# Kernel optimization log

Hardware: AMD Instinct MI355X
Metric: run time of the kernel (lower is better)

Reference implementation:

```python
import jax, jax.numpy as jnp
import numpy as np
import math

B, T, C, H = 4, 2048, 1024, 16
D = C // H  # head dim = 64
W_STD = 0.02


def setup_inputs() -> dict:
    key = jax.random.key(0)
    kx, kw, kb = jax.random.split(key, 3)
    x = jax.random.normal(kx, (B, T, C), dtype=jnp.float32)
    # Linear params stored as [in, 3*in] for x @ W; scaled like typical init
    w_qkv = jax.random.normal(kw, (C, 3 * C), dtype=jnp.float32) * W_STD
    b_qkv = jax.random.normal(kb, (3 * C,), dtype=jnp.float32) * W_STD
    return {"x": x, "w_qkv": w_qkv, "b_qkv": b_qkv}


def reference(x, w_qkv, b_qkv):
    # Fused QKV projection; torch splits as keys, queries, values (in that order)
    qkv = x @ w_qkv + b_qkv                      # [B, T, 3C]
    k, q, v = jnp.split(qkv, 3, axis=-1)          # each [B, T, C]

    def heads(t):  # [B, T, C] -> [B, H, T, D]
        return t.reshape(B, T, H, D).transpose(0, 2, 1, 3)

    k, q, v = heads(k), heads(q), heads(v)
    scale = 1.0 / math.sqrt(D)
    logits = jnp.einsum("bhqd,bhkd->bhqk", q, k) * scale  # [B, H, T, T]
    causal = jnp.tril(jnp.ones((T, T), dtype=bool))
    logits = jnp.where(causal, logits, -jnp.inf)
    probs = jax.nn.softmax(logits, axis=-1)
    y = jnp.einsum("bhqk,bhkd->bhqd", probs, v)   # [B, H, T, D]
    return y.transpose(0, 2, 1, 3).reshape(B, T, C)
```

## Files before the change

### kernel.cpp

```cpp
#include <hip/hip_runtime.h>
#include <hip/hip_bf16.h>

typedef unsigned short ushort_t;
typedef __attribute__((ext_vector_type(4))) short bf16x4_t;
typedef __attribute__((ext_vector_type(8))) short short8;
typedef __attribute__((ext_vector_type(4))) unsigned short ushort4_t;
typedef __attribute__((ext_vector_type(4))) float f32x4;
typedef __attribute__((ext_vector_type(2))) unsigned int uint2_t;
typedef __attribute__((ext_vector_type(4))) unsigned int uint4_t;

#define LOG2E 1.44269504088896340736f

__device__ __forceinline__ unsigned short f2bf(float f) {
    unsigned int u = __float_as_uint(f);
    u += 0x7fffu + ((u >> 16) & 1u);
    return (unsigned short)(u >> 16);
}

__device__ __forceinline__ unsigned int pk2bf(float a, float b) {
    union { __hip_bfloat162 h2; unsigned int u; } cvt;
    cvt.h2 = __float22bfloat162_rn(make_float2(a, b));
    return cvt.u;
}

__device__ __forceinline__ void gl_lds16(const ushort_t* g, ushort_t* l) {
    __builtin_amdgcn_global_load_lds(
        (const __attribute__((address_space(1))) unsigned int*)g,
        (__attribute__((address_space(3))) unsigned int*)l, 16, 0, 0);
}

__device__ __forceinline__ f32x4 mfma16(uint2_t a, uint2_t b, f32x4 c) {
    union { uint2_t u; bf16x4_t s; } ua, ub;
    ua.u = a; ub.u = b;
    return __builtin_amdgcn_mfma_f32_16x16x16bf16_1k(ua.s, ub.s, c, 0, 0, 0);
}

__global__ __launch_bounds__(256) void cvt_x(
    const float* __restrict__ x, ushort_t* __restrict__ xb)
{
    const size_t i = ((size_t)blockIdx.x * 256 + threadIdx.x) * 8;
    const float4 a = *(const float4*)(x + i);
    const float4 b = *(const float4*)(x + i + 4);
    uint4_t o;
    o[0] = pk2bf(a.x, a.y); o[1] = pk2bf(a.z, a.w);
    o[2] = pk2bf(b.x, b.y); o[3] = pk2bf(b.z, b.w);
    *(uint4_t*)(xb + i) = o;
}

__global__ __launch_bounds__(256) void cvt_w(
    const float* __restrict__ w, ushort_t* __restrict__ wt)
{
    __shared__ ushort_t Ts[64][40];
    const int k0 = blockIdx.x * 32, n0 = blockIdx.y * 64;
    const int tid = threadIdx.x;
    const int kr = tid >> 3, nc = (tid & 7) * 8;
    const float* g = w + (size_t)(k0 + kr) * 3072 + n0 + nc;
    const float4 a = *(const float4*)g;
    const float4 b = *(const float4*)(g + 4);
    const float vals[8] = {a.x, a.y, a.z, a.w, b.x, b.y, b.z, b.w};
#pragma unroll
    for (int j = 0; j < 8; ++j) Ts[nc + j][kr] = f2bf(vals[j]);
    __syncthreads();
    const int nr = tid >> 2, kc = (tid & 3) * 8;
    const short8 v = *(const short8*)&Ts[nr][kc];
    *(short8*)(wt + (size_t)(n0 + nr) * 1024 + k0 + kc) = v;
}

__global__ __launch_bounds__(256) void qkv_gemm(
    const ushort_t* __restrict__ xb, const ushort_t* __restrict__ wt,
    const float* __restrict__ bq,
    ushort_t* __restrict__ kws, ushort_t* __restrict__ qws,
    ushort_t* __restrict__ vws)
{
    __shared__ ushort_t As[128 * 32];
    __shared__ ushort_t Bs[128 * 32];

    const int tid  = threadIdx.x;
    const int m0   = blockIdx.x * 128;
    const int n0   = blockIdx.y * 128;
    const int wv   = tid >> 6;
    const int lane = tid & 63;
    const int qr   = lane & 15;
    const int quad = lane >> 4;
    const int wm   = (wv >> 1) * 64;
    const int wn   = (wv & 1) * 64;

    const int lr   = lane >> 2;
    const int scol = (lane & 3) * 8;
    const ushort_t* gA = xb + (size_t)(m0 + wv*32 + lr) * 1024 + scol;
    const ushort_t* gB = wt + (size_t)(n0 + wv*32 + lr) * 1024 + scol;
    ushort_t* lA = As + wv * 32 * 32;
    ushort_t* lB = Bs + wv * 32 * 32;

    f32x4 acc[4][4];
#pragma unroll
    for (int i = 0; i < 4; ++i)
#pragma unroll
        for (int j = 0; j < 4; ++j) acc[i][j] = (f32x4){0.f, 0.f, 0.f, 0.f};

    for (int k0 = 0; k0 < 1024; k0 += 32) {
        __syncthreads();
        gl_lds16(gA + k0,             lA);
        gl_lds16(gA + k0 + 16 * 1024, lA + 16 * 32);
        gl_lds16(gB + k0,             lB);
        gl_lds16(gB + k0 + 16 * 1024, lB + 16 * 32);
        __syncthreads();

        short8 af[4], bfr[4];
#pragma unroll
        for (int i = 0; i < 4; ++i)
            af[i] = *(const short8*)&As[(wm + i*16 + qr) * 32 + quad * 8];
#pragma unroll
        for (int j = 0; j < 4; ++j)
            bfr[j] = *(const short8*)&Bs[(wn + j*16 + qr) * 32 + quad * 8];
#pragma unroll
        for (int i = 0; i < 4; ++i)
#pragma unroll
            for (int j = 0; j < 4; ++j)
                acc[i][j] = __builtin_amdgcn_mfma_f32_16x16x32_bf16(
                    af[i], bfr[j], acc[i][j], 0, 0, 0);
    }

    const int nbase = n0 + wn;
    const int sec   = nbase >> 10;
    const int h     = (nbase & 1023) >> 6;

    if (sec == 2) {
#pragma unroll
        for (int j = 0; j < 4; ++j) {
            const float bias = bq[nbase + j*16 + qr];
            const int d = j*16 + qr;
#pragma unroll
            for (int i = 0; i < 4; ++i) {
                const int m  = m0 + wm + i*16 + quad*4;
                const int bb = m >> 11;
                const int tt = m & 2047;
                ushort4_t pk;
#pragma unroll
                for (int r = 0; r < 4; ++r) pk[r] = f2bf(acc[i][j][r] + bias);
                *(ushort4_t*)&vws[((size_t)(bb*16 + h)*64 + d)*2048 + tt] = pk;
            }
        }
    } else {
        ushort_t* __restrict__ dst = (sec == 0) ? kws : qws;
#pragma unroll
        for (int j = 0; j < 4; ++j) {
            const float bias = bq[nbase + j*16 + qr];
            const int d = j*16 + qr;
#pragma unroll
            for (int i = 0; i < 4; ++i) {
#pragma unroll
                for (int r = 0; r < 4; ++r) {
                    const int m  = m0 + wm + i*16 + quad*4 + r;
                    const int bb = m >> 11;
                    const int tt = m & 2047;
                    dst[(((size_t)(bb*16 + h)) * 2048 + tt) * 64 + d] =
                        f2bf(acc[i][j][r] + bias);
                }
            }
        }
    }
}

__global__ __launch_bounds__(256) void attn_fwd(
    const ushort_t* __restrict__ kws, const ushort_t* __restrict__ qws,
    const ushort_t* __restrict__ vws, float* __restrict__ out,
    unsigned int* __restrict__ counter)
{
    constexpr int LDK = 72;
    __shared__ ushort_t Ks[2][64 * LDK];
    __shared__ ushort_t Vs[2][64 * LDK];
    __shared__ int s_item;

    const int tid  = threadIdx.x;
    const int wv   = tid >> 6;
    const int lane = tid & 63;
    const int qr   = lane & 15;
    const int quad = lane >> 4;
    const int srow = tid >> 2;
    const int scol = (tid & 3) * 16;
    constexpr float SCL = 0.125f * LOG2E;
    constexpr float CB  = 8.0f;

    for (;;) {
        if (tid == 0) s_item = (int)atomicAdd(counter, 1u);
        __syncthreads();
        const int item = s_item;
        if (item >= 1024) break;

        const int qt = 15 - (item >> 6);
        const int bh = item & 63;
        const int q0 = qt * 128;
        const size_t bhT = (size_t)bh * 2048;
        const ushort_t* kbase = kws + bhT * 64;
        const ushort_t* vbase = vws + (size_t)bh * 64 * 2048;

        const int base = q0 + wv*32;
        const int qv0 = base + qr;
        const int qv1 = qv0 + 16;

        const ushort_t* qg0 = qws + (bhT + qv0) * 64;
        const ushort_t* qg1 = qws + (bhT + qv1) * 64;
        const short8 Qb00 = *(const short8*)(qg0 + quad*8);
        const short8 Qb01 = *(const short8*)(qg0 + 32 + quad*8);
        const short8 Qb10 = *(const short8*)(qg1 + quad*8);
        const short8 Qb11 = *(const short8*)(qg1 + 32 + quad*8);

        float l_s[2] = {0.f, 0.f};
        f32x4 Oacc[2][4];
#pragma unroll
        for (int qs = 0; qs < 2; ++qs)
#pragma unroll
            for (int dt = 0; dt < 4; ++dt) Oacc[qs][dt] = (f32x4){0.f,0.f,0.f,0.f};

        const int nkt = 2*qt + 2;
        const int row_max = base + 31;

        short8 kv0, kv1, vv0, vv1;
        {
            const ushort_t* kg = kbase + (size_t)srow * 64 + scol;
            const ushort_t* vg = vbase + (size_t)srow * 2048 + scol;
            kv0 = *(const short8*)(kg);     kv1 = *(const short8*)(kg + 8);
            vv0 = *(const short8*)(vg);     vv1 = *(const short8*)(vg + 8);
        }
        *(short8*)&Ks[0][srow * LDK + scol]     = kv0;
        *(short8*)&Ks[0][srow * LDK + scol + 8] = kv1;
        *(short8*)&Vs[0][srow * LDK + scol]     = vv0;
        *(short8*)&Vs[0][srow * LDK + scol + 8] = vv1;
        __syncthreads();

        for (int kt = 0; kt < nkt; ++kt) {
            const int k0 = kt * 64;
            const int cur = kt & 1;
            const bool more = (kt + 1 < nkt);
            if (more) {
                const ushort_t* kg = kbase + (size_t)(k0 + 64 + srow) * 64 + scol;
                const ushort_t* vg = vbase + (size_t)srow * 2048 + k0 + 64 + scol;
                kv0 = *(const short8*)(kg);   kv1 = *(const short8*)(kg + 8);
                vv0 = *(const short8*)(vg);   vv1 = *(const short8*)(vg + 8);
            }

            if (k0 <= row_max) {
                const ushort_t* Kc = Ks[cur];
                const ushort_t* Vc = Vs[cur];
                const bool diag = (k0 + 63 > base);

                uint2_t pks[2][4];
                float ps0 = 0.f, ps1 = 0.f;
#pragma unroll
                for (int t4 = 0; t4 < 4; ++t4) {
                    const short8 kf0 = *(const short8*)&Kc[(t4*16 + qr)*LDK + quad*8];
                    const short8 kf1 = *(const short8*)&Kc[(t4*16 + qr)*LDK + 32 + quad*8];
                    f32x4 a = (f32x4){0.f,0.f,0.f,0.f};
                    f32x4 b = (f32x4){0.f,0.f,0.f,0.f};
                    a = __builtin_amdgcn_mfma_f32_16x16x32_bf16(kf0, Qb00, a, 0,0,0);
                    a = __builtin_amdgcn_mfma_f32_16x16x32_bf16(kf1, Qb01, a, 0,0,0);
                    b = __builtin_amdgcn_mfma_f32_16x16x32_bf16(kf0, Qb10, b, 0,0,0);
                    b = __builtin_amdgcn_mfma_f32_16x16x32_bf16(kf1, Qb11, b, 0,0,0);
                    if (diag) {
#pragma unroll
                        for (int r = 0; r < 4; ++r) {
                            const int key = k0 + t4*16 + quad*4 + r;
                            if (key > qv0) a[r] = -INFINITY;
                            if (key > qv1) b[r] = -INFINITY;
                        }
                    }
                    float p0[4], p1[4];
#pragma unroll
                    for (int r = 0; r < 4; ++r) {
                        p0[r] = exp2f(__builtin_fmaf(a[r], SCL, -CB));
                        p1[r] = exp2f(__builtin_fmaf(b[r], SCL, -CB));
                        ps0 += p0[r];
                        ps1 += p1[r];
                    }
                    pks[0][t4][0] = pk2bf(p0[0], p0[1]);
                    pks[0][t4][1] = pk2bf(p0[2], p0[3]);
                    pks[1][t4][0] = pk2bf(p1[0], p1[1]);
                    pks[1][t4][1] = pk2bf(p1[2], p1[3]);
                }
                l_s[0] += ps0;
                l_s[1] += ps1;

#pragma unroll
                for (int dt = 0; dt < 4; ++dt) {
#pragma unroll
                    for (int t4 = 0; t4 < 4; ++t4) {
                        const uint2_t vf = *(const uint2_t*)
                            &Vc[(dt*16 + qr)*LDK + t4*16 + quad*4];
                        Oacc[0][dt] = mfma16(pks[0][t4], vf, Oacc[0][dt]);
                        Oacc[1][dt] = mfma16(pks[1][t4], vf, Oacc[1][dt]);
                    }
                }
            }

            if (more) {
                ushort_t* Kn = Ks[cur ^ 1];
                ushort_t* Vn = Vs[cur ^ 1];
                *(short8*)&Kn[srow * LDK + scol]     = kv0;
                *(short8*)&Kn[srow * LDK + scol + 8] = kv1;
                *(short8*)&Vn[srow * LDK + scol]     = vv0;
                *(short8*)&Vn[srow * LDK + scol + 8] = vv1;
            }
            __syncthreads();
        }

        const int b = bh >> 4, h = bh & 15;
#pragma unroll
        for (int qs = 0; qs < 2; ++qs) {
            float lf = l_s[qs];
            lf += __shfl_xor(lf, 16);
            lf += __shfl_xor(lf, 32);
#pragma unroll
            for (int r = 0; r < 4; ++r) {
                const float lr  = __shfl(lf, quad*4 + r);
                const float inv = 1.f / lr;
                const int q = q0 + wv*32 + qs*16 + quad*4 + r;
                float* o = out + ((size_t)(b*2048 + q)) * 1024 + h*64;
#pragma unroll
                for (int dt = 0; dt < 4; ++dt) o[dt*16 + qr] = Oacc[qs][dt][r] * inv;
            }
        }
    }
}

extern "C" void kernel_launch(void* const* d_in, const int* in_sizes, int n_in,
                              void* d_out, int out_size, void* d_ws, size_t ws_size,
                              hipStream_t stream) {
    (void)in_sizes; (void)n_in; (void)out_size; (void)ws_size;
    const float* x  = (const float*)d_in[0];
    const float* w  = (const float*)d_in[1];
    const float* bq = (const float*)d_in[2];
    float* out = (float*)d_out;

    ushort_t* kws = (ushort_t*)d_ws;
    ushort_t* qws = kws + (size_t)8388608;
    ushort_t* vws = qws + (size_t)8388608;
    ushort_t* xb  = vws + (size_t)8388608;
    ushort_t* wt  = xb  + (size_t)8388608;
    unsigned int* counter = (unsigned int*)(wt + (size_t)3145728);

    (void)hipMemsetAsync(counter, 0, 4, stream);
    cvt_x<<<4096, 256, 0, stream>>>(x, xb);
    cvt_w<<<dim3(32, 48), 256, 0, stream>>>(w, wt);
    qkv_gemm<<<dim3(64, 24), 256, 0, stream>>>(xb, wt, bq, kws, qws, vws);
    attn_fwd<<<1024, 256, 0, stream>>>(kws, qws, vws, out, counter);
}
```

Baseline: 264.0 us.

## Replace atomic work queue with static paired causal tiles per block

The attention kernel no longer pulls work items from an atomic counter. Each of 512 blocks statically handles two query tiles (jp and 15-jp) of one batch-head, so every block gets the same causal workload. This drops the memset, the per-item atomic and the barrier, and may improve K/V cache locality within a head. In exchange there is no dynamic balancing, and with 512 equal blocks the tail depends on how they map onto the CUs.

Result: faster. 248.3 us (-5.9%).

```diff
diff --git a/kernel.cpp b/kernel.cpp
--- a/kernel.cpp
+++ b/kernel.cpp
@@ -164,13 +164,11 @@
 
 __global__ __launch_bounds__(256) void attn_fwd(
     const ushort_t* __restrict__ kws, const ushort_t* __restrict__ qws,
-    const ushort_t* __restrict__ vws, float* __restrict__ out,
-    unsigned int* __restrict__ counter)
+    const ushort_t* __restrict__ vws, float* __restrict__ out)
 {
     constexpr int LDK = 72;
     __shared__ ushort_t Ks[2][64 * LDK];
     __shared__ ushort_t Vs[2][64 * LDK];
-    __shared__ int s_item;
 
     const int tid  = threadIdx.x;
     const int wv   = tid >> 6;
@@ -182,18 +180,17 @@
     constexpr float SCL = 0.125f * LOG2E;
     constexpr float CB  = 8.0f;
 
-    for (;;) {
-        if (tid == 0) s_item = (int)atomicAdd(counter, 1u);
-        __syncthreads();
-        const int item = s_item;
-        if (item >= 1024) break;
-
-        const int qt = 15 - (item >> 6);
-        const int bh = item & 63;
+    const int bh = (int)blockIdx.x >> 3;
+    const int jp = (int)blockIdx.x & 7;
+    const size_t bhT = (size_t)bh * 2048;
+    const ushort_t* kbase = kws + bhT * 64;
+    const ushort_t* vbase = vws + (size_t)bh * 64 * 2048;
+    const int b = bh >> 4, h = bh & 15;
+
+#pragma unroll 1
+    for (int part = 0; part < 2; ++part) {
+        const int qt = part ? (15 - jp) : jp;
         const int q0 = qt * 128;
-        const size_t bhT = (size_t)bh * 2048;
-        const ushort_t* kbase = kws + bhT * 64;
-        const ushort_t* vbase = vws + (size_t)bh * 64 * 2048;
 
         const int base = q0 + wv*32;
         const int qv0 = base + qr;
@@ -252,24 +249,24 @@
                     const short8 kf0 = *(const short8*)&Kc[(t4*16 + qr)*LDK + quad*8];
                     const short8 kf1 = *(const short8*)&Kc[(t4*16 + qr)*LDK + 32 + quad*8];
                     f32x4 a = (f32x4){0.f,0.f,0.f,0.f};
-                    f32x4 b = (f32x4){0.f,0.f,0.f,0.f};
-                    a = __builtin_amdgcn_mfma_f32_16x16x32_bf16(kf0, Qb00, a, 0,0,0);
-                    a = __builtin_amdgcn_mfma_f32_16x16x32_bf16(kf1, Qb01, a, 0,0,0);
-                    b = __builtin_amdgcn_mfma_f32_16x16x32_bf16(kf0, Qb10, b, 0,0,0);
-                    b = __builtin_amdgcn_mfma_f32_16x16x32_bf16(kf1, Qb11, b, 0,0,0);
+                    f32x4 bfr = (f32x4){0.f,0.f,0.f,0.f};
+                    a   = __builtin_amdgcn_mfma_f32_16x16x32_bf16(kf0, Qb00, a, 0,0,0);
+                    a   = __builtin_amdgcn_mfma_f32_16x16x32_bf16(kf1, Qb01, a, 0,0,0);
+                    bfr = __builtin_amdgcn_mfma_f32_16x16x32_bf16(kf0, Qb10, bfr, 0,0,0);
+                    bfr = __builtin_amdgcn_mfma_f32_16x16x32_bf16(kf1, Qb11, bfr, 0,0,0);
                     if (diag) {
 #pragma unroll
                         for (int r = 0; r < 4; ++r) {
                             const int key = k0 + t4*16 + quad*4 + r;
-                            if (key > qv0) a[r] = -INFINITY;
-                            if (key > qv1) b[r] = -INFINITY;
+                            if (key > qv0) a[r]   = -INFINITY;
+                            if (key > qv1) bfr[r] = -INFINITY;
                         }
                     }
                     float p0[4], p1[4];
 #pragma unroll
                     for (int r = 0; r < 4; ++r) {
-                        p0[r] = exp2f(__builtin_fmaf(a[r], SCL, -CB));
-                        p1[r] = exp2f(__builtin_fmaf(b[r], SCL, -CB));
+                        p0[r] = exp2f(__builtin_fmaf(a[r],   SCL, -CB));
+                        p1[r] = exp2f(__builtin_fmaf(bfr[r], SCL, -CB));
                         ps0 += p0[r];
                         ps1 += p1[r];
                     }
@@ -304,7 +301,6 @@
             __syncthreads();
         }
 
-        const int b = bh >> 4, h = bh & 15;
 #pragma unroll
         for (int qs = 0; qs < 2; ++qs) {
             float lf = l_s[qs];
@@ -337,11 +333,9 @@
     ushort_t* vws = qws + (size_t)8388608;
     ushort_t* xb  = vws + (size_t)8388608;
     ushort_t* wt  = xb  + (size_t)8388608;
-    unsigned int* counter = (unsigned int*)(wt + (size_t)3145728);
-
-    (void)hipMemsetAsync(counter, 0, 4, stream);
+
     cvt_x<<<4096, 256, 0, stream>>>(x, xb);
     cvt_w<<<dim3(32, 48), 256, 0, stream>>>(w, wt);
     qkv_gemm<<<dim3(64, 24), 256, 0, stream>>>(xb, wt, bq, kws, qws, vws);
-    attn_fwd<<<1024, 256, 0, stream>>>(kws, qws, vws, out, counter);
-}
+    attn_fwd<<<512, 256, 0, stream>>>(kws, qws, vws, out);
+}
```
